# Performance work log

Measured on AMD Instinct MI355X. Metric: run time of the kernel, lower is better.

Reference implementation:

```python
import jax, jax.numpy as jnp
import numpy as np

EPS = 1e-6
KH = KW = 3  # square kernel the 5-point plus stencil unpacks into


def setup_inputs() -> dict:
    key = jax.random.key(0)
    k1, k2, k3 = jax.random.split(key, 3)
    bs, ci, co, H, W = 8, 256, 256, 128, 128
    x = jax.random.normal(k1, (bs, ci, H, W), dtype=jnp.float32)
    y = jax.random.normal(k2, (bs, ci), dtype=jnp.float32)
    # packed stencil weights (channels_out, channels_in, stencil_size)
    weights = jax.random.normal(k3, (co, ci, 5), dtype=jnp.float32) * 0.02
    # flat indices into the 3x3 kernel for stencil pts (0,1),(1,0),(1,1),(1,2),(2,1)
    stencil_index = jnp.array([1, 3, 4, 5, 7], dtype=jnp.int32)
    return {"x": x, "y": y, "weights": weights, "stencil_index": stencil_index}


def _modulated_lattice_conv(x, y, weights, stencil_index):
    bs, ci, H, W = x.shape
    co = weights.shape[0]
    # StyleGAN2-style modulation: w2 * (w1 + 1)  -> [bs, co, ci, S]
    w = weights[None, :, :, :] * (y[:, None, :, None] + 1.0)
    # demodulation: rsqrt of sum over (in, stencil) dims
    d = jax.lax.rsqrt(jnp.sum(w * w, axis=(2, 3), keepdims=True) + EPS)
    w = w * d
    # fold batch into output channels for groups=batch trick
    w = w.reshape(bs * co, ci, -1)
    # unpack non-square stencil into zero-padded square kernel (irregular scatter)
    full = jnp.zeros((bs * co, ci, KH * KW), dtype=w.dtype)
    full = full.at[:, :, stencil_index].set(w)
    kern = full.reshape(bs * co, ci, KH, KW)
    # grouped conv: input reshaped to (1, bs*ci, H, W), feature_group_count=bs
    out = jax.lax.conv_general_dilated(
        x.reshape(1, bs * ci, H, W), kern,
        window_strides=(1, 1), padding='SAME',
        feature_group_count=bs,
        dimension_numbers=('NCHW', 'OIHW', 'NCHW'))
    return out.reshape(bs, co, H, W)


def reference(x, y, weights, stencil_index):
    return _modulated_lattice_conv(x, y, weights, stencil_index)
```

## Files before the change

kernel.cpp:

```cpp
#include <hip/hip_runtime.h>


typedef short v8s __attribute__((ext_vector_type(8)));
typedef float v4f __attribute__((ext_vector_type(4)));
typedef int   v4i __attribute__((ext_vector_type(4)));

#define BS 8
#define CI 256
#define CO 256
#define HH 128
#define WW 128

#define WF_CK 10240
#define RSTR_B 5632
#define RSTR_I 1408
#define XBUF_I (6 * RSTR_I)
#define XBUF_B (6 * RSTR_B)

#define GLOAD_LDS16(g, l)                                                  \
    __builtin_amdgcn_global_load_lds(                                      \
        (__attribute__((address_space(1))) void*)(g),                      \
        (__attribute__((address_space(3))) void*)(l), 16, 0, 0)

__device__ __forceinline__ unsigned short f2bf(float f) {
    unsigned u = __builtin_bit_cast(unsigned, f);
    u += 0x7FFFu + ((u >> 16) & 1u);
    return (unsigned short)(u >> 16);
}

__global__ __launch_bounds__(256) void prep_kernel(const float* __restrict__ x,
                                                   const float* __restrict__ y,
                                                   const float* __restrict__ wgt,
                                                   short* __restrict__ wfrag,
                                                   unsigned int* __restrict__ xt) {
    __shared__ float tr[32 * 132];
    __shared__ float red[4];

    if (blockIdx.x < 2048) {
        const int bo = blockIdx.x;
        const int b = bo >> 8, o = bo & 255;
        const int ci = threadIdx.x;
        const float ym = y[b * CI + ci] + 1.0f;
        const float* wp = wgt + (o * CI + ci) * 5;
        float w[5];
        float s2 = 0.f;
        #pragma unroll
        for (int s = 0; s < 5; ++s) { w[s] = wp[s]; s2 += w[s] * w[s]; }
        float ss = ym * ym * s2;
        #pragma unroll
        for (int off = 32; off > 0; off >>= 1) ss += __shfl_down(ss, off);
        if ((threadIdx.x & 63) == 0) red[threadIdx.x >> 6] = ss;
        __syncthreads();
        const float tot = red[0] + red[1] + red[2] + red[3];
        const float scale = ym * rsqrtf(tot + 1e-6f);
        const int ot = o >> 6, mt = (o >> 4) & 3, m = o & 15;
        const int ck = ci >> 5, quad = (ci >> 3) & 3, j = ci & 7;
        size_t base = ((size_t)(b * 4 + ot) * 8 + ck) * WF_CK + quad * 128 + m * 8 + j;
        #pragma unroll
        for (int s = 0; s < 5; ++s)
            wfrag[base + (size_t)(s * 4 + mt) * 512] = (short)f2bf(w[s] * scale);
    } else {
        const int bid = blockIdx.x - 2048;
        const int b  = bid >> 10;
        const int ck = (bid >> 7) & 7;
        const int h  = bid & 127;
        const int tid = threadIdx.x;
        #pragma unroll
        for (int i = 0; i < 4; ++i) {
            int q  = tid + i * 256;
            int c  = q >> 5;
            int qp = q & 31;
            v4f v = *(const v4f*)&x[((size_t)(b * CI + ck * 32 + c) * HH + h) * WW
                                    + qp * 4];
            *(v4f*)&tr[c * 132 + qp * 4] = v;
        }
        __syncthreads();
        const int px = tid >> 1, half = tid & 1;
        unsigned pk[8];
        #pragma unroll
        for (int k = 0; k < 8; ++k) {
            float f0 = tr[(half * 16 + 2 * k)     * 132 + px];
            float f1 = tr[(half * 16 + 2 * k + 1) * 132 + px];
            pk[k] = (unsigned)f2bf(f0) | ((unsigned)f2bf(f1) << 16);
        }
        unsigned int* dst = xt + ((size_t)((b * 8 + ck) * 16384 + h * 128 + px)) * 16
                               + half * 8;
        *(v4i*)dst       = (v4i){(int)pk[0], (int)pk[1], (int)pk[2], (int)pk[3]};
        *(v4i*)(dst + 4) = (v4i){(int)pk[4], (int)pk[5], (int)pk[6], (int)pk[7]};
    }
}

__global__ __launch_bounds__(256) void wprep2_kernel(const float* __restrict__ y,
                                                     const float* __restrict__ wgt,
                                                     short* __restrict__ wfrag) {
    const int bo = blockIdx.x;
    const int b = bo >> 8, o = bo & 255;
    const int ci = threadIdx.x;
    const float ym = y[b * CI + ci] + 1.0f;
    const float* wp = wgt + (o * CI + ci) * 5;
    float w[5];
    float s2 = 0.f;
    #pragma unroll
    for (int s = 0; s < 5; ++s) { w[s] = wp[s]; s2 += w[s] * w[s]; }
    float ss = ym * ym * s2;
    #pragma unroll
    for (int off = 32; off > 0; off >>= 1) ss += __shfl_down(ss, off);
    __shared__ float red[4];
    if ((threadIdx.x & 63) == 0) red[threadIdx.x >> 6] = ss;
    __syncthreads();
    const float tot = red[0] + red[1] + red[2] + red[3];
    const float scale = ym * rsqrtf(tot + 1e-6f);
    const int ot = o >> 6, mt = (o >> 4) & 3, m = o & 15;
    const int ck = ci >> 5, quad = (ci >> 3) & 3, j = ci & 7;
    size_t base = ((size_t)(b * 4 + ot) * 8 + ck) * WF_CK + quad * 128 + m * 8 + j;
    #pragma unroll
    for (int s = 0; s < 5; ++s)
        wfrag[base + (size_t)(s * 4 + mt) * 512] = (short)f2bf(w[s] * scale);
}

__global__ __launch_bounds__(256, 2) void conv3_kernel(const char* __restrict__ xt,
                                                       const short* __restrict__ wfrag,
                                                       float* __restrict__ out) {
    const int b     = blockIdx.z;
    const int ot    = blockIdx.y;
    const int oBase = ot * 64;
    const int st    = blockIdx.x;
    const int r0    = (st >> 1) * 4;
    const int c0    = (st & 1) * 64;
    const bool left = (c0 == 0);

    const int tid  = threadIdx.x;
    const int wid  = tid >> 6;
    const int lane = tid & 63;
    const int l15  = lane & 15;
    const int quad = lane >> 4;

    __shared__ __align__(16) int xs[2 * XBUF_I];

    v4f acc[4][4];
    #pragma unroll
    for (int a = 0; a < 4; ++a)
        #pragma unroll
        for (int n = 0; n < 4; ++n) acc[a][n] = (v4f){0.f, 0.f, 0.f, 0.f};

    const int row = r0 + wid;
    const short* wfb = wfrag + (size_t)(b * 4 + ot) * 8 * WF_CK;
    const int gstartB = (c0 - 1) * 64;

    const bool rzm  = (!left) && (l15 == 15);
    const bool lzm  = left && (l15 == 0);
    const bool topz = (r0 == 0)      && (wid == 0);
    const bool botz = (r0 == HH - 4) && (wid == 3);
    const v4i z4 = (v4i){0, 0, 0, 0};

    const int dh[5] = {-1, 0, 0, 0, 1};
    const int dw[5] = { 0,-1, 0, 1, 0};

    int goff[8], loff[8];
    #pragma unroll
    for (int k = 0; k < 8; ++k) {
        int q  = wid + 4 * k;
        int qq = q < 30 ? q : q - 2;
        int rr = qq / 5, t = qq - rr * 5;
        int gr = r0 - 1 + rr;
        gr = gr < 0 ? 0 : (gr > 127 ? 127 : gr);
        int l  = t * 64 + lane;
        int gx = l ^ ((l >> 3) & 7);
        goff[k] = gr * 8192 + gstartB + gx * 16;
        loff[k] = rr * RSTR_B + l * 16;
    }

    int boff[5][4];
    #pragma unroll
    for (int s = 0; s < 5; ++s) {
        const int xrow = wid + 1 + dh[s];
        const int xc0  = 1 + dw[s];
        #pragma unroll
        for (int nt = 0; nt < 4; ++nt) {
            int slot = nt * 16 + l15 + xc0;
            int gran = slot * 4 + quad;
            int sg   = gran ^ ((gran >> 3) & 7);
            boff[s][nt] = xrow * RSTR_I + sg * 4;
        }
    }

    auto stage = [&](int ckk, int bufsel) {
        const char* planep = xt + (((size_t)(b * 8 + ckk)) << 20);
        char* lbase = (char*)xs + bufsel * XBUF_B;
        #pragma unroll
        for (int k = 0; k < 8; ++k)
            GLOAD_LDS16(planep + goff[k], lbase + loff[k]);
    };

    v8s af[20];
    auto load_af = [&](int ck) {
        const short* wfc = wfb + (size_t)ck * WF_CK;
        #pragma unroll
        for (int sm = 0; sm < 20; ++sm)
            af[sm] = *(const v8s*)(wfc + (size_t)(sm * 4 + quad) * 128 + l15 * 8);
    };

    auto conv_step = [&](const int* xb) {
        #pragma unroll
        for (int s = 0; s < 5; ++s) {
            #pragma unroll
            for (int nt = 0; nt < 4; ++nt) {
                v4i bi = *(const v4i*)&xb[boff[s][nt]];
                if (s == 0)            { if (topz) bi = z4; }
                if (s == 4)            { if (botz) bi = z4; }
                if (s == 1 && nt == 0) { if (lzm)  bi = z4; }
                if (s == 3 && nt == 3) { if (rzm)  bi = z4; }
                v8s bfr = __builtin_bit_cast(v8s, bi);
                #pragma unroll
                for (int mt = 0; mt < 4; ++mt)
                    acc[mt][nt] = __builtin_amdgcn_mfma_f32_16x16x32_bf16(
                        af[s * 4 + mt], bfr, acc[mt][nt], 0, 0, 0);
            }
        }
    };

    stage(0, 0);
    for (int ck = 0; ck < 7; ++ck) {
        load_af(ck);
        asm volatile("s_waitcnt vmcnt(20)" ::: "memory");
        __builtin_amdgcn_s_barrier();
        stage(ck + 1, (ck + 1) & 1);
        asm volatile("s_waitcnt vmcnt(8)" ::: "memory");
        conv_step(xs + (ck & 1) * XBUF_I);
    }
    load_af(7);
    asm volatile("s_waitcnt vmcnt(20)" ::: "memory");
    __builtin_amdgcn_s_barrier();
    asm volatile("s_waitcnt vmcnt(0)" ::: "memory");
    conv_step(xs + XBUF_I);

    #pragma unroll
    for (int mt = 0; mt < 4; ++mt)
        #pragma unroll
        for (int nt = 0; nt < 4; ++nt)
            #pragma unroll
            for (int r = 0; r < 4; ++r) {
                int o = oBase + mt * 16 + quad * 4 + r;
                int c = c0 + nt * 16 + l15;
                out[((size_t)(b * CO + o) * HH + row) * WW + c] = acc[mt][nt][r];
            }
}

__global__ __launch_bounds__(256, 4) void conv_kernel(const float* __restrict__ x,
                                                      const short* __restrict__ wfrag,
                                                      float* __restrict__ out) {
    const int b     = blockIdx.z;
    const int ot    = blockIdx.y;
    const int oBase = ot * 64;
    const int st    = blockIdx.x;
    const int r0    = (st >> 1) * 4;
    const int c0    = (st & 1) * 64;
    const int tid  = threadIdx.x;
    const int wid  = tid >> 6;
    const int lane = tid & 63;
    const int l15  = lane & 15;
    const int quad = lane >> 4;
    #define PXS 20
    __shared__ __align__(16) int xs[6 * 66 * PXS];
    v4f acc[4][4];
    #pragma unroll
    for (int a = 0; a < 4; ++a)
        #pragma unroll
        for (int n = 0; n < 4; ++n) acc[a][n] = (v4f){0.f, 0.f, 0.f, 0.f};
    const int row = r0 + wid;
    const short* wfb = wfrag + (size_t)(b * 4 + ot) * 8 * WF_CK;
    const int dh[5] = {-1, 0, 0, 0, 1};
    const int dw[5] = { 0,-1, 0, 1, 0};
    for (int ck = 0; ck < 8; ++ck) {
        const int ic0 = ck * 32;
        #pragma unroll
        for (int t = 0; t < 6; ++t) {
            int idx = tid + t * 256;
            int cp  = idx & 15;
            int tmp = idx >> 4;
            int cq  = tmp & 15;
            int rr  = tmp >> 4;
            int gr  = r0 - 1 + rr;
            v4f a0 = (v4f){0.f, 0.f, 0.f, 0.f}, a1 = a0;
            if (gr >= 0 && gr < HH) {
                const float* xp = x + ((size_t)(b * CI + ic0 + cp * 2) * HH + gr) * WW
                                    + (c0 + cq * 4);
                a0 = *(const v4f*)xp;
                a1 = *(const v4f*)(xp + HH * WW);
            }
            int base = (rr * 66 + cq * 4 + 1) * PXS + cp;
            #pragma unroll
            for (int k = 0; k < 4; ++k)
                xs[base + k * PXS] =
                    (int)((unsigned)f2bf(a0[k]) | ((unsigned)f2bf(a1[k]) << 16));
        }
        if (tid < 192) {
            int cp   = tid & 15;
            int tmp  = tid >> 4;
            int side = (tmp >= 6) ? 1 : 0;
            int rr   = tmp - 6 * side;
            int gr   = r0 - 1 + rr;
            int gc   = side ? (c0 + 64) : (c0 - 1);
            float v0 = 0.f, v1 = 0.f;
            if (gr >= 0 && gr < HH && gc >= 0 && gc < WW) {
                const float* xp = x + ((size_t)(b * CI + ic0 + cp * 2) * HH + gr) * WW + gc;
                v0 = xp[0];
                v1 = xp[HH * WW];
            }
            int col = side ? 65 : 0;
            xs[(rr * 66 + col) * PXS + cp] =
                (int)((unsigned)f2bf(v0) | ((unsigned)f2bf(v1) << 16));
        }
        __syncthreads();
        const short* wfc = wfb + (size_t)ck * WF_CK;
        #pragma unroll
        for (int s = 0; s < 5; ++s) {
            const int xrow = wid + 1 + dh[s];
            const int xc0  = 1 + dw[s];
            v8s af[4];
            #pragma unroll
            for (int mt = 0; mt < 4; ++mt)
                af[mt] = *(const v8s*)(wfc + (size_t)((s * 4 + mt) * 4 + quad) * 128
                                           + l15 * 8);
            #pragma unroll
            for (int nt = 0; nt < 4; ++nt) {
                int px = xrow * 66 + nt * 16 + l15 + xc0;
                v4i bi = *(const v4i*)&xs[px * PXS + quad * 4];
                v8s bfr = __builtin_bit_cast(v8s, bi);
                #pragma unroll
                for (int mt = 0; mt < 4; ++mt)
                    acc[mt][nt] = __builtin_amdgcn_mfma_f32_16x16x32_bf16(
                        af[mt], bfr, acc[mt][nt], 0, 0, 0);
            }
        }
        __syncthreads();
    }
    #pragma unroll
    for (int mt = 0; mt < 4; ++mt)
        #pragma unroll
        for (int nt = 0; nt < 4; ++nt)
            #pragma unroll
            for (int r = 0; r < 4; ++r) {
                int o = oBase + mt * 16 + quad * 4 + r;
                int c = c0 + nt * 16 + l15;
                out[((size_t)(b * CO + o) * HH + row) * WW + c] = acc[mt][nt][r];
            }
}

__global__ __launch_bounds__(256) void demod_kernel(const float* __restrict__ y,
                                                    const float* __restrict__ wgt,
                                                    float* __restrict__ dbuf) {
    const int bo = blockIdx.x;
    const int b = bo >> 8, o = bo & 255;
    const int i = threadIdx.x;
    const float* wp = wgt + (o * CI + i) * 5;
    const float ym = y[b * CI + i] + 1.0f;
    float s2 = 0.f;
    #pragma unroll
    for (int s = 0; s < 5; ++s) { float w = wp[s]; s2 += w * w; }
    float val = ym * ym * s2;
    #pragma unroll
    for (int off = 32; off > 0; off >>= 1) val += __shfl_down(val, off);
    __shared__ float red[4];
    if ((threadIdx.x & 63) == 0) red[threadIdx.x >> 6] = val;
    __syncthreads();
    if (threadIdx.x == 0) dbuf[bo] = rsqrtf(red[0] + red[1] + red[2] + red[3] + 1e-6f);
}

__global__ __launch_bounds__(256) void conv_kernel_fb(const float* __restrict__ x,
                                                      const float* __restrict__ y,
                                                      const float* __restrict__ wgt,
                                                      const float* __restrict__ dbuf,
                                                      float* __restrict__ out) {
    const int b     = blockIdx.z;
    const int oBase = blockIdx.y * 64;
    const int st    = blockIdx.x;
    const int r0    = (st >> 1) * 4;
    const int c0    = (st & 1) * 64;
    const int tid  = threadIdx.x;
    const int wid  = tid >> 6;
    const int lane = tid & 63;
    const int l15  = lane & 15;
    const int quad = lane >> 4;
    __shared__ int   xs4[16 * 412];
    __shared__ short wlds[5 * 4 * 4 * 16 * 8];
    v4f acc[4][4];
    #pragma unroll
    for (int a = 0; a < 4; ++a)
        #pragma unroll
        for (int n = 0; n < 4; ++n) acc[a][n] = (v4f){0.f, 0.f, 0.f, 0.f};
    const int row = r0 + wid;
    for (int ic0 = 0; ic0 < CI; ic0 += 32) {
        for (int t = 0; t < 25; ++t) {
            int idx = tid + t * 256;
            if (idx < 6336) {
                int cp  = idx / 396;
                int rem = idx - cp * 396;
                int rr  = rem / 66;
                int cc  = rem - rr * 66;
                int gr  = r0 - 1 + rr;
                int gc  = c0 - 1 + cc;
                float v0 = 0.f, v1 = 0.f;
                if (gr >= 0 && gr < HH && gc >= 0 && gc < WW) {
                    const float* xp = x + ((size_t)(b * CI + ic0 + cp * 2) * HH + gr) * WW + gc;
                    v0 = xp[0];
                    v1 = xp[HH * WW];
                }
                xs4[cp * 412 + rr * 68 + cc] =
                    (int)((unsigned)f2bf(v0) | ((unsigned)f2bf(v1) << 16));
            }
        }
        #pragma unroll
        for (int p = 0; p < 8; ++p) {
            int pidx = tid + p * 256;
            int ol = pidx >> 5;
            int il = pidx & 31;
            int o  = oBase + ol;
            int ci = ic0 + il;
            float scale = (y[b * CI + ci] + 1.0f) * dbuf[b * CO + o];
            const float* wp = wgt + (o * CI + ci) * 5;
            int base = (((ol >> 4) * 4 + (il >> 3)) * 16 + (ol & 15)) * 8 + (il & 7);
            #pragma unroll
            for (int s = 0; s < 5; ++s)
                wlds[base + s * (4 * 4 * 16 * 8)] = (short)f2bf(wp[s] * scale);
        }
        __syncthreads();
        const int dh[5] = {-1, 0, 0, 0, 1};
        const int dw[5] = { 0,-1, 0, 1, 0};
        #pragma unroll
        for (int s = 0; s < 5; ++s) {
            int xrow = wid + 1 + dh[s];
            int xcb  = l15 + 1 + dw[s];
            v8s af[4];
            #pragma unroll
            for (int mt = 0; mt < 4; ++mt)
                af[mt] = *(const v8s*)&wlds[(((s * 4 + mt) * 4 + quad) * 16 + l15) * 8];
            #pragma unroll
            for (int nt = 0; nt < 4; ++nt) {
                v4i bi;
                #pragma unroll
                for (int p = 0; p < 4; ++p)
                    bi[p] = xs4[(quad * 4 + p) * 412 + xrow * 68 + nt * 16 + xcb];
                v8s bfr = __builtin_bit_cast(v8s, bi);
                #pragma unroll
                for (int mt = 0; mt < 4; ++mt)
                    acc[mt][nt] = __builtin_amdgcn_mfma_f32_16x16x32_bf16(
                        af[mt], bfr, acc[mt][nt], 0, 0, 0);
            }
        }
        __syncthreads();
    }
    #pragma unroll
    for (int mt = 0; mt < 4; ++mt)
        #pragma unroll
        for (int nt = 0; nt < 4; ++nt)
            #pragma unroll
            for (int r = 0; r < 4; ++r) {
                int o = oBase + mt * 16 + quad * 4 + r;
                int c = c0 + nt * 16 + l15;
                out[((size_t)(b * CO + o) * HH + row) * WW + c] = acc[mt][nt][r];
            }
}

extern "C" void kernel_launch(void* const* d_in, const int* in_sizes, int n_in,
                              void* d_out, int out_size, void* d_ws, size_t ws_size,
                              hipStream_t stream) {
    const float* x   = (const float*)d_in[0];
    const float* y   = (const float*)d_in[1];
    const float* wgt = (const float*)d_in[2];
    float* out = (float*)d_out;

    const size_t WF_BYTES = (size_t)BS * 4 * 8 * WF_CK * sizeof(short);
    const size_t XT_OFF   = WF_BYTES + 8192;
    const size_t XT_BYTES = (size_t)BS * 8 * 16384 * 64;
    const size_t NEED_FULL = XT_OFF + XT_BYTES + 1024;
    const size_t NEED_MID  = WF_BYTES + 8192;

    short* wfrag = (short*)d_ws;

    if (ws_size >= NEED_FULL) {
        unsigned int* xt = (unsigned int*)((char*)d_ws + XT_OFF);
        prep_kernel<<<dim3(2048 + BS * 8 * HH), dim3(256), 0, stream>>>(
            x, y, wgt, wfrag, xt);
        conv3_kernel<<<dim3(64, CO / 64, BS), dim3(256), 0, stream>>>(
            (const char*)xt, wfrag, out);
    } else if (ws_size >= NEED_MID) {
        wprep2_kernel<<<dim3(BS * CO), dim3(256), 0, stream>>>(y, wgt, wfrag);
        conv_kernel<<<dim3(64, CO / 64, BS), dim3(256), 0, stream>>>(x, wfrag, out);
    } else {
        float* dbuf = (float*)d_ws;
        demod_kernel<<<dim3(BS * CO), dim3(256), 0, stream>>>(y, wgt, dbuf);
        conv_kernel_fb<<<dim3(64, CO / 64, BS), dim3(256), 0, stream>>>(x, y, wgt, dbuf, out);
    }
}
```

Before: 310.7 us.

## Restructure conv3 main loop into per-stencil phases with split staging and remapped grid

Splits each channel-chunk step into five stencil phases. Each phase prefetches the next phase's weight fragments, issues half of the next chunk's global-to-LDS staging in the first two phases, and raises wave priority around the MFMA block. This replaces holding all 20 weight fragments in registers, which lowers register pressure but adds two barriers per phase. It also switches the LDS layout from the XOR swizzle to a quad-major layout with a smaller row stride, and remaps block indices so neighbouring blocks spread across batch and output tiles. The new layout could bring back LDS bank conflicts, and the extra barriers add synchronisation cost.

```diff
diff --git a/kernel.cpp b/kernel.cpp
--- a/kernel.cpp
+++ b/kernel.cpp
@@ -12,10 +12,9 @@
 #define WW 128
 
 #define WF_CK 10240
-#define RSTR_B 5632
-#define RSTR_I 1408
-#define XBUF_I (6 * RSTR_I)
-#define XBUF_B (6 * RSTR_B)
+#define R7STR_B 5120
+#define XB7_I 7680
+#define XB7_B 30720
 
 #define GLOAD_LDS16(g, l)                                                  \
     __builtin_amdgcn_global_load_lds(                                      \
@@ -118,13 +117,55 @@
         wfrag[base + (size_t)(s * 4 + mt) * 512] = (short)f2bf(w[s] * scale);
 }
 
+
+#define PHASE(S, STG, WFN, SN)                                                 \
+  {                                                                            \
+    v8s pafN[4];                                                               \
+    _Pragma("unroll")                                                          \
+    for (int mt = 0; mt < 4; ++mt)                                             \
+      pafN[mt] = *(const v8s*)((WFN) + (size_t)(((SN) * 4 + mt) * 4 + quad)    \
+                                           * 128 + l15 * 8);                   \
+    v4i bi[4];                                                                 \
+    _Pragma("unroll")                                                          \
+    for (int nt = 0; nt < 4; ++nt)                                             \
+      bi[nt] = *(const v4i*)&xb[boff_i[(S)][nt]];                              \
+    if ((STG) == 1) stage4(ckn, bufn, 0);                                      \
+    if ((STG) == 2) stage4(ckn, bufn, 4);                                      \
+    __builtin_amdgcn_sched_barrier(0);                                         \
+    __builtin_amdgcn_s_barrier();                                              \
+    __builtin_amdgcn_sched_barrier(0);                                         \
+    if ((S) == 0) { if (topz) { bi[0] = z4; bi[1] = z4; bi[2] = z4; bi[3] = z4; } } \
+    if ((S) == 4) { if (botz) { bi[0] = z4; bi[1] = z4; bi[2] = z4; bi[3] = z4; } } \
+    if ((S) == 1) { if (lzm) bi[0] = z4; }                                     \
+    if ((S) == 3) { if (rzm) bi[3] = z4; }                                     \
+    __builtin_amdgcn_s_setprio(1);                                             \
+    _Pragma("unroll")                                                          \
+    for (int nt = 0; nt < 4; ++nt) {                                           \
+      v8s bfr = __builtin_bit_cast(v8s, bi[nt]);                               \
+      _Pragma("unroll")                                                        \
+      for (int mt = 0; mt < 4; ++mt)                                           \
+        acc[mt][nt] = __builtin_amdgcn_mfma_f32_16x16x32_bf16(                 \
+            pafC[mt], bfr, acc[mt][nt], 0, 0, 0);                              \
+    }                                                                          \
+    __builtin_amdgcn_s_setprio(0);                                             \
+    if ((S) == 4) {                                                            \
+      __builtin_amdgcn_sched_barrier(0);                                       \
+      asm volatile("s_waitcnt vmcnt(0)" ::: "memory");                         \
+    }                                                                          \
+    __builtin_amdgcn_s_barrier();                                              \
+    _Pragma("unroll")                                                          \
+    for (int mt = 0; mt < 4; ++mt) pafC[mt] = pafN[mt];                        \
+  }
+
 __global__ __launch_bounds__(256, 2) void conv3_kernel(const char* __restrict__ xt,
                                                        const short* __restrict__ wfrag,
                                                        float* __restrict__ out) {
-    const int b     = blockIdx.z;
-    const int ot    = blockIdx.y;
+    const int flat = blockIdx.x + 64 * (blockIdx.y + 4 * blockIdx.z);
+    const int wrk  = (flat & 7) * 256 + (flat >> 3);
+    const int b    = wrk >> 8;
+    const int ot   = (wrk >> 6) & 3;
+    const int st   = wrk & 63;
     const int oBase = ot * 64;
-    const int st    = blockIdx.x;
     const int r0    = (st >> 1) * 4;
     const int c0    = (st & 1) * 64;
     const bool left = (c0 == 0);
@@ -135,7 +176,7 @@
     const int l15  = lane & 15;
     const int quad = lane >> 4;
 
-    __shared__ __align__(16) int xs[2 * XBUF_I];
+    __shared__ __align__(16) int xs[2 * XB7_I];
 
     v4f acc[4][4];
     #pragma unroll
@@ -162,77 +203,65 @@
         int q  = wid + 4 * k;
         int qq = q < 30 ? q : q - 2;
         int rr = qq / 5, t = qq - rr * 5;
+        int g  = t * 64 + lane;
+        int qd = g / 80, px = g - qd * 80;
         int gr = r0 - 1 + rr;
         gr = gr < 0 ? 0 : (gr > 127 ? 127 : gr);
-        int l  = t * 64 + lane;
-        int gx = l ^ ((l >> 3) & 7);
-        goff[k] = gr * 8192 + gstartB + gx * 16;
-        loff[k] = rr * RSTR_B + l * 16;
-    }
-
-    int boff[5][4];
+        goff[k] = gr * 8192 + gstartB + px * 64 + qd * 16;
+        loff[k] = rr * R7STR_B + g * 16;
+    }
+
+    int boff_i[5][4];
     #pragma unroll
     for (int s = 0; s < 5; ++s) {
         const int xrow = wid + 1 + dh[s];
         const int xc0  = 1 + dw[s];
         #pragma unroll
-        for (int nt = 0; nt < 4; ++nt) {
-            int slot = nt * 16 + l15 + xc0;
-            int gran = slot * 4 + quad;
-            int sg   = gran ^ ((gran >> 3) & 7);
-            boff[s][nt] = xrow * RSTR_I + sg * 4;
-        }
-    }
-
-    auto stage = [&](int ckk, int bufsel) {
+        for (int nt = 0; nt < 4; ++nt)
+            boff_i[s][nt] = xrow * 1280 + quad * 320 + (nt * 16 + l15 + xc0) * 4;
+    }
+
+    auto stage4 = [&](int ckk, int bufsel, int k0) {
         const char* planep = xt + (((size_t)(b * 8 + ckk)) << 20);
-        char* lbase = (char*)xs + bufsel * XBUF_B;
-        #pragma unroll
-        for (int k = 0; k < 8; ++k)
-            GLOAD_LDS16(planep + goff[k], lbase + loff[k]);
+        char* lbase = (char*)xs + bufsel * XB7_B;
+        #pragma unroll
+        for (int kk = 0; kk < 4; ++kk)
+            GLOAD_LDS16(planep + goff[k0 + kk], lbase + loff[k0 + kk]);
     };
 
-    v8s af[20];
-    auto load_af = [&](int ck) {
-        const short* wfc = wfb + (size_t)ck * WF_CK;
-        #pragma unroll
-        for (int sm = 0; sm < 20; ++sm)
-            af[sm] = *(const v8s*)(wfc + (size_t)(sm * 4 + quad) * 128 + l15 * 8);
-    };
-
-    auto conv_step = [&](const int* xb) {
-        #pragma unroll
-        for (int s = 0; s < 5; ++s) {
-            #pragma unroll
-            for (int nt = 0; nt < 4; ++nt) {
-                v4i bi = *(const v4i*)&xb[boff[s][nt]];
-                if (s == 0)            { if (topz) bi = z4; }
-                if (s == 4)            { if (botz) bi = z4; }
-                if (s == 1 && nt == 0) { if (lzm)  bi = z4; }
-                if (s == 3 && nt == 3) { if (rzm)  bi = z4; }
-                v8s bfr = __builtin_bit_cast(v8s, bi);
-                #pragma unroll
-                for (int mt = 0; mt < 4; ++mt)
-                    acc[mt][nt] = __builtin_amdgcn_mfma_f32_16x16x32_bf16(
-                        af[s * 4 + mt], bfr, acc[mt][nt], 0, 0, 0);
-            }
-        }
-    };
-
-    stage(0, 0);
+    stage4(0, 0, 0);
+    stage4(0, 0, 4);
+    v8s pafC[4];
+    #pragma unroll
+    for (int mt = 0; mt < 4; ++mt)
+        pafC[mt] = *(const v8s*)(wfb + (size_t)(mt * 4 + quad) * 128 + l15 * 8);
+    asm volatile("s_waitcnt vmcnt(0)" ::: "memory");
+    __builtin_amdgcn_s_barrier();
+
     for (int ck = 0; ck < 7; ++ck) {
-        load_af(ck);
-        asm volatile("s_waitcnt vmcnt(20)" ::: "memory");
-        __builtin_amdgcn_s_barrier();
-        stage(ck + 1, (ck + 1) & 1);
-        asm volatile("s_waitcnt vmcnt(8)" ::: "memory");
-        conv_step(xs + (ck & 1) * XBUF_I);
-    }
-    load_af(7);
-    asm volatile("s_waitcnt vmcnt(20)" ::: "memory");
-    __builtin_amdgcn_s_barrier();
-    asm volatile("s_waitcnt vmcnt(0)" ::: "memory");
-    conv_step(xs + XBUF_I);
+        const short* wfc  = wfb + (size_t)ck * WF_CK;
+        const short* wfcN = wfc + WF_CK;
+        const int*   xb   = xs + (ck & 1) * XB7_I;
+        const int    bufn = (ck + 1) & 1;
+        const int    ckn  = ck + 1;
+        PHASE(0, 1, wfc, 1)
+        PHASE(1, 2, wfc, 2)
+        PHASE(2, 0, wfc, 3)
+        PHASE(3, 0, wfc, 4)
+        PHASE(4, 0, wfcN, 0)
+    }
+    {
+        const short* wfc  = wfb + (size_t)7 * WF_CK;
+        const int*   xb   = xs + XB7_I;
+        const int    bufn = 0;
+        const int    ckn  = 0;
+        (void)bufn; (void)ckn;
+        PHASE(0, 0, wfc, 1)
+        PHASE(1, 0, wfc, 2)
+        PHASE(2, 0, wfc, 3)
+        PHASE(3, 0, wfc, 4)
+        PHASE(4, 0, wfc, 0)
+    }
 
     #pragma unroll
     for (int mt = 0; mt < 4; ++mt)
```

New measurement: 329.8 us. +6.1%, slower.
